# Performance work log

Hardware: AMD Instinct MI355X
Metric: run time of the kernel (lower is better)

## Reference

```python
import jax, jax.numpy as jnp
import numpy as np

N, D, H = 4096, 1024, 8
HD = D // H
FFN = int(D * 1.5)
TAU_NEG = 0.6
BETA = 1.5
LN_EPS = 1e-5


def _layernorm(x, g, b):
    mu = jnp.mean(x, axis=-1, keepdims=True)
    var = jnp.mean((x - mu) ** 2, axis=-1, keepdims=True)
    return (x - mu) * jax.lax.rsqrt(var + LN_EPS) * g + b


def setup_inputs() -> dict:
    key = jax.random.key(0)
    ks = jax.random.split(key, 16)
    s = 0.02
    inp = {
        "features": jax.random.normal(ks[0], (N, D), jnp.float32),
        "coords": jax.random.randint(ks[1], (N, 2), 0, 128, jnp.int32),
        "Wq": jax.random.normal(ks[2], (D, D), jnp.float32) * s,
        "Wk": jax.random.normal(ks[3], (D, D), jnp.float32) * s,
        "Wv": jax.random.normal(ks[4], (D, D), jnp.float32) * s,
        "Wo": jax.random.normal(ks[5], (D, D), jnp.float32) * s,
        "bo": jnp.zeros((D,), jnp.float32),
        "ln1_g": jnp.ones((D,), jnp.float32),
        "ln1_b": jnp.zeros((D,), jnp.float32),
        "W1": jax.random.normal(ks[6], (FFN, D), jnp.float32) * s,
        "b1": jnp.zeros((FFN,), jnp.float32),
        "W2": jax.random.normal(ks[7], (D, FFN), jnp.float32) * s,
        "b2": jnp.zeros((D,), jnp.float32),
        "ln2_g": jnp.ones((D,), jnp.float32),
        "ln2_b": jnp.zeros((D,), jnp.float32),
    }
    return inp


def reference(features, coords, Wq, Wk, Wv, Wo, bo, ln1_g, ln1_b, W1, b1, W2, b2, ln2_g, ln2_b):
    # QKV projections (torch Linear: x @ W.T), reshape to [H, N, HD]
    Q = (features @ Wq.T).reshape(N, H, HD).transpose(1, 0, 2)
    K = (features @ Wk.T).reshape(N, H, HD).transpose(1, 0, 2)
    V = (features @ Wv.T).reshape(N, H, HD).transpose(1, 0, 2)

    scores = jnp.einsum('hnd,hmd->hnm', Q, K) / jnp.sqrt(jnp.float32(HD))  # [H,N,N]

    # spatial distance bias from barcode coords, scaled per head by 1/2^(h+1)
    c = coords.astype(jnp.float32)
    diff = c[:, None, :] - c[None, :, :]
    dist = jnp.sqrt(jnp.sum(diff ** 2, axis=-1))  # [N,N]
    head_scalings = 1.0 / (2.0 ** (jnp.arange(1, H + 1, dtype=jnp.float32)))
    bias = dist[None, :, :] * head_scalings[:, None, None]  # [H,N,N]

    attn_pos = jax.nn.softmax(scores - bias, axis=-1)
    attn_neg = jax.nn.softmax((-scores - bias) / TAU_NEG, axis=-1)
    attn = attn_pos - BETA * attn_neg  # dropout is identity in eval

    attended = jnp.einsum('hnm,hmd->hnd', attn, V)  # [H,N,HD]
    attended = attended.transpose(1, 0, 2).reshape(N, D)

    x = attended @ Wo.T + bo + features
    x = _layernorm(x, ln1_g, ln1_b)

    h = jax.nn.gelu(x @ W1.T + b1, approximate=False)  # torch default GELU = exact erf
    ffn_out = h @ W2.T + b2
    return _layernorm(ffn_out + x, ln2_g, ln2_b)
```

## Files before the change

### kernel.cpp

```cpp
#include <hip/hip_runtime.h>
#include <cstdint>
#include <cstddef>

#define NTOK 4096
#define DMODEL 1024
#define NHEAD 8
#define DHEAD 128
#define DFFN 1536
#define LNEPS 1e-5f

typedef __bf16 bf16_t;
typedef __bf16 bf16x8 __attribute__((ext_vector_type(8)));
typedef __bf16 bf16x4 __attribute__((ext_vector_type(4)));
typedef float f32x4 __attribute__((ext_vector_type(4)));
typedef float f32x16 __attribute__((ext_vector_type(16)));

__device__ __forceinline__ void gload_lds16(const bf16_t* g, bf16_t* lds) {
  __builtin_amdgcn_global_load_lds(
      (const __attribute__((address_space(1))) unsigned int*)g,
      (__attribute__((address_space(3))) unsigned int*)lds, 16, 0, 0);
}

__device__ __forceinline__ float fexp2(float x) {
  float r;
  asm("v_exp_f32 %0, %1" : "=v"(r) : "v"(x));
  return r;
}
__device__ __forceinline__ float fsqrt(float x) {
  float r;
  asm("v_sqrt_f32 %0, %1" : "=v"(r) : "v"(x));
  return r;
}
__device__ __forceinline__ unsigned cvtpk(float lo, float hi) {
  unsigned r;
  asm("v_cvt_pk_bf16_f32 %0, %1, %2" : "=v"(r) : "v"(lo), "v"(hi));
  return r;
}

__global__ __launch_bounds__(256) void cvt_kernel(const float* __restrict__ in,
                                                  bf16_t* __restrict__ out, int n4) {
  int i = blockIdx.x * 256 + threadIdx.x;
  if (i < n4) {
    const float4 v = reinterpret_cast<const float4*>(in)[i];
    bf16x4 o = {(bf16_t)v.x, (bf16_t)v.y, (bf16_t)v.z, (bf16_t)v.w};
    reinterpret_cast<bf16x4*>(out)[i] = o;
  }
}

__global__ __launch_bounds__(256) void cvtc_kernel(const int* __restrict__ in,
                                                   float2* __restrict__ out, int n) {
  int i = blockIdx.x * 256 + threadIdx.x;
  if (i < n) {
    int2 c = reinterpret_cast<const int2*>(in)[i];
    out[i] = make_float2((float)c.x, (float)c.y);
  }
}

template<int EPI>
__global__ __launch_bounds__(256) void gemm_bt(
    const bf16_t* __restrict__ A, const bf16_t* __restrict__ B,
    int M, int Nn, int K,
    const float* __restrict__ bias, const float* __restrict__ resid,
    float* __restrict__ outF, bf16_t* __restrict__ outH)
{
  __shared__ bf16_t As[64 * 32];
  __shared__ bf16_t Bs[128 * 32];
  const int t = threadIdx.x;
  const int w = t >> 6, l = t & 63;
  const int lg = l >> 4, li = l & 15;
  const int m0 = blockIdx.x * 64, n0 = blockIdx.y * 128;
  const int wr = (w >> 1) * 32, wc = (w & 1) * 64;
  const f32x4 fz = {0.f, 0.f, 0.f, 0.f};
  f32x4 acc[2][4];
#pragma unroll
  for (int i = 0; i < 2; i++)
#pragma unroll
    for (int j = 0; j < 4; j++) acc[i][j] = fz;

  const bf16_t* Ag = A + (size_t)m0 * K;
  const bf16_t* Bg = B + (size_t)n0 * K;

  for (int kt = 0; kt < K; kt += 32) {
    if (kt) __syncthreads();
    {
      int c = w * 64 + l;
      gload_lds16(Ag + (size_t)(c >> 2) * K + kt + (c & 3) * 8,
                  As + (w * 64) * 8);
#pragma unroll
      for (int p = 0; p < 2; p++) {
        int cb = p * 256 + w * 64 + l;
        gload_lds16(Bg + (size_t)(cb >> 2) * K + kt + (cb & 3) * 8,
                    Bs + (p * 256 + w * 64) * 8);
      }
    }
    __syncthreads();
    bf16x8 af[2], bfr[4];
#pragma unroll
    for (int mi = 0; mi < 2; mi++)
      af[mi] = *reinterpret_cast<const bf16x8*>(&As[(wr + mi * 16 + li) * 32 + lg * 8]);
#pragma unroll
    for (int ni = 0; ni < 4; ni++)
      bfr[ni] = *reinterpret_cast<const bf16x8*>(&Bs[(wc + ni * 16 + li) * 32 + lg * 8]);
#pragma unroll
    for (int mi = 0; mi < 2; mi++)
#pragma unroll
      for (int ni = 0; ni < 4; ni++)
        acc[mi][ni] = __builtin_amdgcn_mfma_f32_16x16x32_bf16(af[mi], bfr[ni], acc[mi][ni], 0, 0, 0);
  }

#pragma unroll
  for (int mi = 0; mi < 2; mi++) {
#pragma unroll
    for (int ni = 0; ni < 4; ni++) {
      int gcol = n0 + wc + ni * 16 + li;
#pragma unroll
      for (int r = 0; r < 4; r++) {
        int grow = m0 + wr + mi * 16 + lg * 4 + r;
        float v = acc[mi][ni][r];
        if (EPI == 0) {
          outH[(size_t)grow * Nn + gcol] = (bf16_t)v;
        } else if (EPI == 1) {
          v += bias[gcol] + resid[(size_t)grow * Nn + gcol];
          outF[(size_t)grow * Nn + gcol] = v;
        } else if (EPI == 2) {
          v += bias[gcol];
          v = 0.5f * v * (1.f + erff(v * 0.70710678118654752f));
          outH[(size_t)grow * Nn + gcol] = (bf16_t)v;
        } else {
          v += bias[gcol] + resid[(size_t)grow * Nn + gcol];
          outF[(size_t)grow * Nn + gcol] = v;
        }
      }
    }
  }
}

__global__ __launch_bounds__(256) void packkv_kernel(
    const bf16_t* __restrict__ K, const bf16_t* __restrict__ V,
    bf16_t* __restrict__ Kp, bf16_t* __restrict__ Vp)
{
  const int h = blockIdx.x & 7;
  const int T = blockIdx.x >> 3;
  const int t = threadIdx.x;
  const size_t obase = ((size_t)(h * 128 + T)) * 4096;
#pragma unroll
  for (int rep = 0; rep < 2; rep++) {
    int idx = rep * 256 + t;
    int frag = idx >> 6, l = idx & 63;
    int q5 = l & 31, hi = l >> 5;
    bf16x8 kk = *reinterpret_cast<const bf16x8*>(
        K + (size_t)(T * 32 + q5) * DMODEL + h * DHEAD + frag * 16 + hi * 8);
    *reinterpret_cast<bf16x8*>(Kp + obase + (size_t)idx * 8) = kk;
    int ks = frag >> 2, f = frag & 3;
    bf16x8 vv;
#pragma unroll
    for (int j = 0; j < 8; j++)
      vv[j] = V[(size_t)(T * 32 + ks * 16 + hi * 8 + j) * DMODEL + h * DHEAD + 32 * f + q5];
    *reinterpret_cast<bf16x8*>(Vp + obase + (size_t)idx * 8) = vv;
  }
}

__global__ __launch_bounds__(128, 2) void attn9_kernel(
    const bf16_t* __restrict__ Q, const bf16_t* __restrict__ Kp,
    const bf16_t* __restrict__ Vp, const float2* __restrict__ cf,
    bf16_t* __restrict__ out)
{
  __shared__ float buf[128 * 33];
  __shared__ float mlS[2][32];

  const int t = threadIdx.x;
  const int w = t >> 6;
  const int l = t & 63;
  const int q5 = l & 31;
  const int hi = l >> 5;
  const int h = blockIdx.x & 7;
  const int q0 = (blockIdx.x >> 3) * 32;
  const float LOG2E = 1.44269504088896f;
  const float isq = 0.08838834764831845f;
  const float itau = 1.6666666666666667f;
  const float hs = 1.0f / (float)(2 << h);
  const float ap = isq * LOG2E;
  const float an = -isq * itau * LOG2E;
  const float bpp = hs * LOG2E;

  bf16x8 qf[8];
  {
    const bf16_t* qrow = Q + (size_t)(q0 + q5) * DMODEL + h * DHEAD;
#pragma unroll
    for (int c = 0; c < 8; c++)
      qf[c] = *reinterpret_cast<const bf16x8*>(qrow + c * 16 + hi * 8);
  }
  const float2 qc = cf[q0 + q5];
  const float qxs = qc.x * bpp, qys = qc.y * bpp;

  f32x16 accp[4], accn[4];
#pragma unroll
  for (int f = 0; f < 4; f++) {
#pragma unroll
    for (int r = 0; r < 16; r++) { accp[f][r] = 0.f; accn[f][r] = 0.f; }
  }
  float lp = 0.f, lN = 0.f;

  const bf16_t* kpb = Kp + ((size_t)(h * 128 + w * 64)) * 4096 + l * 8;
  const bf16_t* vpb = Vp + ((size_t)(h * 128 + w * 64)) * 4096 + l * 8;

  for (int it = 0; it < 64; it++) {
    const int kv0 = w * 2048 + it * 32;

    bf16x8 kf[8];
#pragma unroll
    for (int c = 0; c < 8; c++)
      kf[c] = *reinterpret_cast<const bf16x8*>(kpb + (size_t)it * 4096 + c * 512);

    f32x16 sacc, sacc2;
#pragma unroll
    for (int r = 0; r < 16; r++) { sacc[r] = 0.f; sacc2[r] = 0.f; }
#pragma unroll
    for (int c = 0; c < 4; c++) {
      sacc = __builtin_amdgcn_mfma_f32_32x32x16_bf16(kf[2 * c], qf[2 * c], sacc, 0, 0, 0);
      sacc2 = __builtin_amdgcn_mfma_f32_32x32x16_bf16(kf[2 * c + 1], qf[2 * c + 1], sacc2, 0, 0, 0);
    }

    bf16x8 vf[8];
#pragma unroll
    for (int fr = 0; fr < 8; fr++)
      vf[fr] = *reinterpret_cast<const bf16x8*>(vpb + (size_t)it * 4096 + fr * 512);

#pragma unroll
    for (int r = 0; r < 16; r++) sacc[r] += sacc2[r];

    float p16[16], n16[16];
#pragma unroll
    for (int r = 0; r < 16; r++) {
      int kvr = kv0 + (r & 3) + 8 * (r >> 2) + 4 * hi;
      float2 c = cf[kvr];
      float dx = __builtin_fmaf(c.x, -bpp, qxs);
      float dy = __builtin_fmaf(c.y, -bpp, qys);
      float u = fsqrt(__builtin_fmaf(dy, dy, dx * dx));
      float pv = fexp2(__builtin_fmaf(sacc[r], ap, -u));
      float nv = fexp2(__builtin_fmaf(sacc[r], an, u * -itau));
      p16[r] = pv; n16[r] = nv;
      lp += pv; lN += nv;
    }

    unsigned pw[2][4], nw[2][4];
#pragma unroll
    for (int ks = 0; ks < 2; ks++) {
#pragma unroll
      for (int u = 0; u < 2; u++) {
        unsigned A = cvtpk(p16[8 * ks + 2 * u], p16[8 * ks + 2 * u + 1]);
        unsigned B = cvtpk(p16[8 * ks + 4 + 2 * u], p16[8 * ks + 4 + 2 * u + 1]);
        unsigned Ax = __shfl_xor(A, 32, 64);
        unsigned Bx = __shfl_xor(B, 32, 64);
        pw[ks][u] = hi ? Bx : A;
        pw[ks][2 + u] = hi ? B : Ax;
        unsigned C = cvtpk(n16[8 * ks + 2 * u], n16[8 * ks + 2 * u + 1]);
        unsigned D = cvtpk(n16[8 * ks + 4 + 2 * u], n16[8 * ks + 4 + 2 * u + 1]);
        unsigned Cx = __shfl_xor(C, 32, 64);
        unsigned Dx = __shfl_xor(D, 32, 64);
        nw[ks][u] = hi ? Dx : C;
        nw[ks][2 + u] = hi ? D : Cx;
      }
    }

#pragma unroll
    for (int ks = 0; ks < 2; ks++) {
      union { unsigned u[4]; bf16x8 v; } pb, nb;
#pragma unroll
      for (int j = 0; j < 4; j++) { pb.u[j] = pw[ks][j]; nb.u[j] = nw[ks][j]; }
#pragma unroll
      for (int f = 0; f < 4; f++) {
        accp[f] = __builtin_amdgcn_mfma_f32_32x32x16_bf16(vf[ks * 4 + f], pb.v, accp[f], 0, 0, 0);
        accn[f] = __builtin_amdgcn_mfma_f32_32x32x16_bf16(vf[ks * 4 + f], nb.v, accn[f], 0, 0, 0);
      }
    }
  }

  float lpw = lp + __shfl_xor(lp, 32, 64);
  float lnw = lN + __shfl_xor(lN, 32, 64);

  __syncthreads();
  if (w == 1) {
    if (hi == 0) { mlS[0][q5] = lpw; mlS[1][q5] = lnw; }
#pragma unroll
    for (int f = 0; f < 4; f++)
#pragma unroll
      for (int r = 0; r < 16; r++)
        buf[(32 * f + (r & 3) + 8 * (r >> 2) + 4 * hi) * 33 + q5] = accp[f][r];
  }
  __syncthreads();
  float lpt = 0.f, lnt = 0.f;
  if (w == 0) {
    lpt = lpw + mlS[0][q5];
    lnt = lnw + mlS[1][q5];
#pragma unroll
    for (int f = 0; f < 4; f++)
#pragma unroll
      for (int r = 0; r < 16; r++)
        accp[f][r] += buf[(32 * f + (r & 3) + 8 * (r >> 2) + 4 * hi) * 33 + q5];
  }
  __syncthreads();
  if (w == 1) {
#pragma unroll
    for (int f = 0; f < 4; f++)
#pragma unroll
      for (int r = 0; r < 16; r++)
        buf[(32 * f + (r & 3) + 8 * (r >> 2) + 4 * hi) * 33 + q5] = accn[f][r];
  }
  __syncthreads();
  if (w == 0) {
    float ip = 1.f / lpt, inn = 1.5f / lnt;
#pragma unroll
    for (int f = 0; f < 4; f++)
#pragma unroll
      for (int r = 0; r < 16; r++) {
        int row = 32 * f + (r & 3) + 8 * (r >> 2) + 4 * hi;
        float an2 = accn[f][r] + buf[row * 33 + q5];
        buf[row * 33 + q5] = accp[f][r] * ip - an2 * inn;
      }
  }
  __syncthreads();

  {
    int q = t >> 2, dq = (t & 3) * 32;
#pragma unroll
    for (int j = 0; j < 4; j++) {
      bf16x8 ov;
#pragma unroll
      for (int e = 0; e < 8; e++) ov[e] = (bf16_t)buf[(dq + j * 8 + e) * 33 + q];
      *reinterpret_cast<bf16x8*>(out + (size_t)(q0 + q) * DMODEL + h * DHEAD + dq + j * 8) = ov;
    }
  }
}

__global__ __launch_bounds__(256) void ln_kernel(
    const float* __restrict__ in, const float* __restrict__ g, const float* __restrict__ b,
    float* __restrict__ outF, bf16_t* __restrict__ outH)
{
  int row = blockIdx.x, t = threadIdx.x;
  const float4 v = reinterpret_cast<const float4*>(in + (size_t)row * DMODEL)[t];
  float s = v.x + v.y + v.z + v.w;
  float ss = v.x * v.x + v.y * v.y + v.z * v.z + v.w * v.w;
#pragma unroll
  for (int m = 32; m >= 1; m >>= 1) {
    s += __shfl_xor(s, m, 64);
    ss += __shfl_xor(ss, m, 64);
  }
  __shared__ float red[8];
  int w = t >> 6, l = t & 63;
  if (l == 0) { red[w] = s; red[4 + w] = ss; }
  __syncthreads();
  s = red[0] + red[1] + red[2] + red[3];
  ss = red[4] + red[5] + red[6] + red[7];
  float mu = s * (1.f / DMODEL);
  float var = ss * (1.f / DMODEL) - mu * mu;
  float rs = rsqrtf(var + LNEPS);
  const float4 gv = reinterpret_cast<const float4*>(g)[t];
  const float4 bv = reinterpret_cast<const float4*>(b)[t];
  float y0 = (v.x - mu) * rs * gv.x + bv.x;
  float y1 = (v.y - mu) * rs * gv.y + bv.y;
  float y2 = (v.z - mu) * rs * gv.z + bv.z;
  float y3 = (v.w - mu) * rs * gv.w + bv.w;
  if (outF) {
    float4 o; o.x = y0; o.y = y1; o.z = y2; o.w = y3;
    reinterpret_cast<float4*>(outF + (size_t)row * DMODEL)[t] = o;
  }
  if (outH) {
    bf16x4 o = {(bf16_t)y0, (bf16_t)y1, (bf16_t)y2, (bf16_t)y3};
    reinterpret_cast<bf16x4*>(outH + (size_t)row * DMODEL)[t] = o;
  }
}

extern "C" void kernel_launch(void* const* d_in, const int* in_sizes, int n_in,
                              void* d_out, int out_size, void* d_ws, size_t ws_size,
                              hipStream_t stream) {
  (void)in_sizes; (void)n_in; (void)out_size; (void)ws_size;
  const float* features = (const float*)d_in[0];
  const int* coords = (const int*)d_in[1];
  const float* Wq = (const float*)d_in[2];
  const float* Wk = (const float*)d_in[3];
  const float* Wv = (const float*)d_in[4];
  const float* Wo = (const float*)d_in[5];
  const float* bo = (const float*)d_in[6];
  const float* ln1g = (const float*)d_in[7];
  const float* ln1b = (const float*)d_in[8];
  const float* W1 = (const float*)d_in[9];
  const float* b1 = (const float*)d_in[10];
  const float* W2 = (const float*)d_in[11];
  const float* b2 = (const float*)d_in[12];
  const float* ln2g = (const float*)d_in[13];
  const float* ln2b = (const float*)d_in[14];
  float* outp = (float*)d_out;

  char* ws = (char*)d_ws;
  size_t off = 0;
  auto alloc = [&](size_t bytes) -> void* {
    void* p = ws + off;
    off += (bytes + 255) & ~((size_t)255);
    return p;
  };
  bf16_t* fb16 = (bf16_t*)alloc((size_t)NTOK * DMODEL * 2);
  bf16_t* wq16 = (bf16_t*)alloc((size_t)DMODEL * DMODEL * 2);
  bf16_t* wk16 = (bf16_t*)alloc((size_t)DMODEL * DMODEL * 2);
  bf16_t* wv16 = (bf16_t*)alloc((size_t)DMODEL * DMODEL * 2);
  bf16_t* wo16 = (bf16_t*)alloc((size_t)DMODEL * DMODEL * 2);
  bf16_t* w116 = (bf16_t*)alloc((size_t)DFFN * DMODEL * 2);
  bf16_t* w216 = (bf16_t*)alloc((size_t)DMODEL * DFFN * 2);
  bf16_t* q16 = (bf16_t*)alloc((size_t)NTOK * DMODEL * 2);
  bf16_t* k16 = (bf16_t*)alloc((size_t)NTOK * DMODEL * 2);
  bf16_t* v16 = (bf16_t*)alloc((size_t)NTOK * DMODEL * 2);
  float* acc1 = (float*)alloc((size_t)NTOK * DMODEL * 4);
  float* xf = (float*)alloc((size_t)NTOK * DMODEL * 4);
  bf16_t* x16 = (bf16_t*)alloc((size_t)NTOK * DMODEL * 2);
  bf16_t* h16 = (bf16_t*)alloc((size_t)NTOK * DFFN * 2);
  float2* cfl = (float2*)alloc((size_t)NTOK * sizeof(float2));
  bf16_t* att16 = fb16;
  bf16_t* Kp = (bf16_t*)acc1;
  bf16_t* Vp = (bf16_t*)h16;

  cvt_kernel<<<dim3(NTOK * DMODEL / 1024), 256, 0, stream>>>(features, fb16, NTOK * DMODEL / 4);
  cvt_kernel<<<dim3(DMODEL * DMODEL / 1024), 256, 0, stream>>>(Wq, wq16, DMODEL * DMODEL / 4);
  cvt_kernel<<<dim3(DMODEL * DMODEL / 1024), 256, 0, stream>>>(Wk, wk16, DMODEL * DMODEL / 4);
  cvt_kernel<<<dim3(DMODEL * DMODEL / 1024), 256, 0, stream>>>(Wv, wv16, DMODEL * DMODEL / 4);
  cvt_kernel<<<dim3(DMODEL * DMODEL / 1024), 256, 0, stream>>>(Wo, wo16, DMODEL * DMODEL / 4);
  cvt_kernel<<<dim3(DFFN * DMODEL / 1024), 256, 0, stream>>>(W1, w116, DFFN * DMODEL / 4);
  cvt_kernel<<<dim3(DMODEL * DFFN / 1024), 256, 0, stream>>>(W2, w216, DMODEL * DFFN / 4);
  cvtc_kernel<<<dim3(NTOK / 256), 256, 0, stream>>>(coords, cfl, NTOK);

  dim3 gQKV(NTOK / 64, DMODEL / 128);
  gemm_bt<0><<<gQKV, 256, 0, stream>>>(fb16, wq16, NTOK, DMODEL, DMODEL, nullptr, nullptr, nullptr, q16);
  gemm_bt<0><<<gQKV, 256, 0, stream>>>(fb16, wk16, NTOK, DMODEL, DMODEL, nullptr, nullptr, nullptr, k16);
  gemm_bt<0><<<gQKV, 256, 0, stream>>>(fb16, wv16, NTOK, DMODEL, DMODEL, nullptr, nullptr, nullptr, v16);
  packkv_kernel<<<dim3(NTOK / 32 * NHEAD), 256, 0, stream>>>(k16, v16, Kp, Vp);
  attn9_kernel<<<dim3(NTOK / 32 * NHEAD), 128, 0, stream>>>(q16, Kp, Vp, cfl, att16);
  gemm_bt<1><<<gQKV, 256, 0, stream>>>(att16, wo16, NTOK, DMODEL, DMODEL, bo, features, acc1, nullptr);
  ln_kernel<<<dim3(NTOK), 256, 0, stream>>>(acc1, ln1g, ln1b, xf, x16);
  gemm_bt<2><<<dim3(NTOK / 64, DFFN / 128), 256, 0, stream>>>(x16, w116, NTOK, DFFN, DMODEL, b1, nullptr, nullptr, h16);
  gemm_bt<3><<<gQKV, 256, 0, stream>>>(h16, w216, NTOK, DMODEL, DFFN, b2, xf, acc1, nullptr);
  ln_kernel<<<dim3(NTOK), 256, 0, stream>>>(acc1, ln2g, ln2b, outp, nullptr);
}
```

Before: 340.9 us.

## Fuse QKV GEMMs with K/V packing epilogue and double-buffer GEMM LDS

Concatenates Wq/Wk/Wv into one weight buffer and runs a single QKV GEMM whose epilogue writes Q row-major and scatters K and V straight into the packed per-head layouts the attention kernel expects. This removes the separate packkv pass and its extra read and write of K and V. All GEMMs also get double-buffered LDS tiles, so the next K-slice load can overlap the MFMA work on the current one. In exchange, the epilogue stores become scattered scalar writes, LDS use doubles, and Kp/Vp now get their own workspace instead of aliasing acc1 and h16.

```diff
diff --git a/kernel.cpp b/kernel.cpp
--- a/kernel.cpp
+++ b/kernel.cpp
@@ -63,8 +63,8 @@
     const float* __restrict__ bias, const float* __restrict__ resid,
     float* __restrict__ outF, bf16_t* __restrict__ outH)
 {
-  __shared__ bf16_t As[64 * 32];
-  __shared__ bf16_t Bs[128 * 32];
+  __shared__ bf16_t As[2][64 * 32];
+  __shared__ bf16_t Bs[2][128 * 32];
   const int t = threadIdx.x;
   const int w = t >> 6, l = t & 63;
   const int lg = l >> 4, li = l & 15;
@@ -79,33 +79,43 @@
 
   const bf16_t* Ag = A + (size_t)m0 * K;
   const bf16_t* Bg = B + (size_t)n0 * K;
-
-  for (int kt = 0; kt < K; kt += 32) {
-    if (kt) __syncthreads();
-    {
-      int c = w * 64 + l;
-      gload_lds16(Ag + (size_t)(c >> 2) * K + kt + (c & 3) * 8,
-                  As + (w * 64) * 8);
+  const int ca = w * 64 + l;
+  const int nK = K >> 5;
+
+  gload_lds16(Ag + (size_t)(ca >> 2) * K + (ca & 3) * 8, &As[0][(w * 64) * 8]);
+#pragma unroll
+  for (int p = 0; p < 2; p++) {
+    int cb = p * 256 + ca;
+    gload_lds16(Bg + (size_t)(cb >> 2) * K + (cb & 3) * 8, &Bs[0][(p * 256 + w * 64) * 8]);
+  }
+  __syncthreads();
+
+  for (int ki = 0; ki < nK; ki++) {
+    const int cur = ki & 1;
+    if (ki + 1 < nK) {
+      const int kt = (ki + 1) << 5;
+      gload_lds16(Ag + (size_t)(ca >> 2) * K + kt + (ca & 3) * 8,
+                  &As[cur ^ 1][(w * 64) * 8]);
 #pragma unroll
       for (int p = 0; p < 2; p++) {
-        int cb = p * 256 + w * 64 + l;
+        int cb = p * 256 + ca;
         gload_lds16(Bg + (size_t)(cb >> 2) * K + kt + (cb & 3) * 8,
-                    Bs + (p * 256 + w * 64) * 8);
-      }
-    }
-    __syncthreads();
+                    &Bs[cur ^ 1][(p * 256 + w * 64) * 8]);
+      }
+    }
     bf16x8 af[2], bfr[4];
 #pragma unroll
     for (int mi = 0; mi < 2; mi++)
-      af[mi] = *reinterpret_cast<const bf16x8*>(&As[(wr + mi * 16 + li) * 32 + lg * 8]);
+      af[mi] = *reinterpret_cast<const bf16x8*>(&As[cur][(wr + mi * 16 + li) * 32 + lg * 8]);
 #pragma unroll
     for (int ni = 0; ni < 4; ni++)
-      bfr[ni] = *reinterpret_cast<const bf16x8*>(&Bs[(wc + ni * 16 + li) * 32 + lg * 8]);
+      bfr[ni] = *reinterpret_cast<const bf16x8*>(&Bs[cur][(wc + ni * 16 + li) * 32 + lg * 8]);
 #pragma unroll
     for (int mi = 0; mi < 2; mi++)
 #pragma unroll
       for (int ni = 0; ni < 4; ni++)
         acc[mi][ni] = __builtin_amdgcn_mfma_f32_16x16x32_bf16(af[mi], bfr[ni], acc[mi][ni], 0, 0, 0);
+    __syncthreads();
   }
 
 #pragma unroll
@@ -135,28 +145,94 @@
   }
 }
 
-__global__ __launch_bounds__(256) void packkv_kernel(
-    const bf16_t* __restrict__ K, const bf16_t* __restrict__ V,
-    bf16_t* __restrict__ Kp, bf16_t* __restrict__ Vp)
+__global__ __launch_bounds__(256) void gemm_qkv(
+    const bf16_t* __restrict__ A, const bf16_t* __restrict__ B,
+    bf16_t* __restrict__ Qo, bf16_t* __restrict__ Kp, bf16_t* __restrict__ Vp)
 {
-  const int h = blockIdx.x & 7;
-  const int T = blockIdx.x >> 3;
+  const int K = DMODEL;
+  __shared__ bf16_t As[2][64 * 32];
+  __shared__ bf16_t Bs[2][128 * 32];
   const int t = threadIdx.x;
-  const size_t obase = ((size_t)(h * 128 + T)) * 4096;
-#pragma unroll
-  for (int rep = 0; rep < 2; rep++) {
-    int idx = rep * 256 + t;
-    int frag = idx >> 6, l = idx & 63;
-    int q5 = l & 31, hi = l >> 5;
-    bf16x8 kk = *reinterpret_cast<const bf16x8*>(
-        K + (size_t)(T * 32 + q5) * DMODEL + h * DHEAD + frag * 16 + hi * 8);
-    *reinterpret_cast<bf16x8*>(Kp + obase + (size_t)idx * 8) = kk;
-    int ks = frag >> 2, f = frag & 3;
-    bf16x8 vv;
-#pragma unroll
-    for (int j = 0; j < 8; j++)
-      vv[j] = V[(size_t)(T * 32 + ks * 16 + hi * 8 + j) * DMODEL + h * DHEAD + 32 * f + q5];
-    *reinterpret_cast<bf16x8*>(Vp + obase + (size_t)idx * 8) = vv;
+  const int w = t >> 6, l = t & 63;
+  const int lg = l >> 4, li = l & 15;
+  const int m0 = blockIdx.x * 64, n0 = blockIdx.y * 128;
+  const int wr = (w >> 1) * 32, wc = (w & 1) * 64;
+  const f32x4 fz = {0.f, 0.f, 0.f, 0.f};
+  f32x4 acc[2][4];
+#pragma unroll
+  for (int i = 0; i < 2; i++)
+#pragma unroll
+    for (int j = 0; j < 4; j++) acc[i][j] = fz;
+
+  const bf16_t* Ag = A + (size_t)m0 * K;
+  const bf16_t* Bg = B + (size_t)n0 * K;
+  const int ca = w * 64 + l;
+  const int nK = K >> 5;
+
+  gload_lds16(Ag + (size_t)(ca >> 2) * K + (ca & 3) * 8, &As[0][(w * 64) * 8]);
+#pragma unroll
+  for (int p = 0; p < 2; p++) {
+    int cb = p * 256 + ca;
+    gload_lds16(Bg + (size_t)(cb >> 2) * K + (cb & 3) * 8, &Bs[0][(p * 256 + w * 64) * 8]);
+  }
+  __syncthreads();
+
+  for (int ki = 0; ki < nK; ki++) {
+    const int cur = ki & 1;
+    if (ki + 1 < nK) {
+      const int kt = (ki + 1) << 5;
+      gload_lds16(Ag + (size_t)(ca >> 2) * K + kt + (ca & 3) * 8,
+                  &As[cur ^ 1][(w * 64) * 8]);
+#pragma unroll
+      for (int p = 0; p < 2; p++) {
+        int cb = p * 256 + ca;
+        gload_lds16(Bg + (size_t)(cb >> 2) * K + kt + (cb & 3) * 8,
+                    &Bs[cur ^ 1][(p * 256 + w * 64) * 8]);
+      }
+    }
+    bf16x8 af[2], bfr[4];
+#pragma unroll
+    for (int mi = 0; mi < 2; mi++)
+      af[mi] = *reinterpret_cast<const bf16x8*>(&As[cur][(wr + mi * 16 + li) * 32 + lg * 8]);
+#pragma unroll
+    for (int ni = 0; ni < 4; ni++)
+      bfr[ni] = *reinterpret_cast<const bf16x8*>(&Bs[cur][(wc + ni * 16 + li) * 32 + lg * 8]);
+#pragma unroll
+    for (int mi = 0; mi < 2; mi++)
+#pragma unroll
+      for (int ni = 0; ni < 4; ni++)
+        acc[mi][ni] = __builtin_amdgcn_mfma_f32_16x16x32_bf16(af[mi], bfr[ni], acc[mi][ni], 0, 0, 0);
+    __syncthreads();
+  }
+
+  const int region = n0 >> 10;
+#pragma unroll
+  for (int mi = 0; mi < 2; mi++) {
+#pragma unroll
+    for (int ni = 0; ni < 4; ni++) {
+      int gcol = n0 + wc + ni * 16 + li;
+#pragma unroll
+      for (int r = 0; r < 4; r++) {
+        int token = m0 + wr + mi * 16 + lg * 4 + r;
+        bf16_t v = (bf16_t)acc[mi][ni][r];
+        if (region == 0) {
+          Qo[(size_t)token * DMODEL + gcol] = v;
+        } else if (region == 1) {
+          int gc = gcol - 1024;
+          int h = gc >> 7, d = gc & 127;
+          size_t addr = ((size_t)(h * 128 + (token >> 5))) * 4096 +
+                        (d >> 4) * 512 + ((d >> 3) & 1) * 256 + (token & 31) * 8 + (d & 7);
+          Kp[addr] = v;
+        } else {
+          int gc = gcol - 2048;
+          int h = gc >> 7, dh = gc & 127;
+          size_t addr = ((size_t)(h * 128 + (token >> 5))) * 4096 +
+                        (((token >> 4) & 1) * 4 + (dh >> 5)) * 512 +
+                        ((token >> 3) & 1) * 256 + (dh & 31) * 8 + (token & 7);
+          Vp[addr] = v;
+        }
+      }
+    }
   }
 }
 
@@ -400,42 +476,35 @@
     return p;
   };
   bf16_t* fb16 = (bf16_t*)alloc((size_t)NTOK * DMODEL * 2);
-  bf16_t* wq16 = (bf16_t*)alloc((size_t)DMODEL * DMODEL * 2);
-  bf16_t* wk16 = (bf16_t*)alloc((size_t)DMODEL * DMODEL * 2);
-  bf16_t* wv16 = (bf16_t*)alloc((size_t)DMODEL * DMODEL * 2);
+  bf16_t* wqkv16 = (bf16_t*)alloc((size_t)3 * DMODEL * DMODEL * 2);
   bf16_t* wo16 = (bf16_t*)alloc((size_t)DMODEL * DMODEL * 2);
   bf16_t* w116 = (bf16_t*)alloc((size_t)DFFN * DMODEL * 2);
   bf16_t* w216 = (bf16_t*)alloc((size_t)DMODEL * DFFN * 2);
   bf16_t* q16 = (bf16_t*)alloc((size_t)NTOK * DMODEL * 2);
-  bf16_t* k16 = (bf16_t*)alloc((size_t)NTOK * DMODEL * 2);
-  bf16_t* v16 = (bf16_t*)alloc((size_t)NTOK * DMODEL * 2);
+  bf16_t* Kp = (bf16_t*)alloc((size_t)NTOK * DMODEL * 2);
+  bf16_t* Vp = (bf16_t*)alloc((size_t)NTOK * DMODEL * 2);
   float* acc1 = (float*)alloc((size_t)NTOK * DMODEL * 4);
   float* xf = (float*)alloc((size_t)NTOK * DMODEL * 4);
   bf16_t* x16 = (bf16_t*)alloc((size_t)NTOK * DMODEL * 2);
   bf16_t* h16 = (bf16_t*)alloc((size_t)NTOK * DFFN * 2);
   float2* cfl = (float2*)alloc((size_t)NTOK * sizeof(float2));
   bf16_t* att16 = fb16;
-  bf16_t* Kp = (bf16_t*)acc1;
-  bf16_t* Vp = (bf16_t*)h16;
 
   cvt_kernel<<<dim3(NTOK * DMODEL / 1024), 256, 0, stream>>>(features, fb16, NTOK * DMODEL / 4);
-  cvt_kernel<<<dim3(DMODEL * DMODEL / 1024), 256, 0, stream>>>(Wq, wq16, DMODEL * DMODEL / 4);
-  cvt_kernel<<<dim3(DMODEL * DMODEL / 1024), 256, 0, stream>>>(Wk, wk16, DMODEL * DMODEL / 4);
-  cvt_kernel<<<dim3(DMODEL * DMODEL / 1024), 256, 0, stream>>>(Wv, wv16, DMODEL * DMODEL / 4);
+  cvt_kernel<<<dim3(DMODEL * DMODEL / 1024), 256, 0, stream>>>(Wq, wqkv16, DMODEL * DMODEL / 4);
+  cvt_kernel<<<dim3(DMODEL * DMODEL / 1024), 256, 0, stream>>>(Wk, wqkv16 + (size_t)DMODEL * DMODEL, DMODEL * DMODEL / 4);
+  cvt_kernel<<<dim3(DMODEL * DMODEL / 1024), 256, 0, stream>>>(Wv, wqkv16 + (size_t)2 * DMODEL * DMODEL, DMODEL * DMODEL / 4);
   cvt_kernel<<<dim3(DMODEL * DMODEL / 1024), 256, 0, stream>>>(Wo, wo16, DMODEL * DMODEL / 4);
   cvt_kernel<<<dim3(DFFN * DMODEL / 1024), 256, 0, stream>>>(W1, w116, DFFN * DMODEL / 4);
   cvt_kernel<<<dim3(DMODEL * DFFN / 1024), 256, 0, stream>>>(W2, w216, DMODEL * DFFN / 4);
   cvtc_kernel<<<dim3(NTOK / 256), 256, 0, stream>>>(coords, cfl, NTOK);
 
-  dim3 gQKV(NTOK / 64, DMODEL / 128);
-  gemm_bt<0><<<gQKV, 256, 0, stream>>>(fb16, wq16, NTOK, DMODEL, DMODEL, nullptr, nullptr, nullptr, q16);
-  gemm_bt<0><<<gQKV, 256, 0, stream>>>(fb16, wk16, NTOK, DMODEL, DMODEL, nullptr, nullptr, nullptr, k16);
-  gemm_bt<0><<<gQKV, 256, 0, stream>>>(fb16, wv16, NTOK, DMODEL, DMODEL, nullptr, nullptr, nullptr, v16);
-  packkv_kernel<<<dim3(NTOK / 32 * NHEAD), 256, 0, stream>>>(k16, v16, Kp, Vp);
+  gemm_qkv<<<dim3(NTOK / 64, 3 * DMODEL / 128), 256, 0, stream>>>(fb16, wqkv16, q16, Kp, Vp);
   attn9_kernel<<<dim3(NTOK / 32 * NHEAD), 128, 0, stream>>>(q16, Kp, Vp, cfl, att16);
-  gemm_bt<1><<<gQKV, 256, 0, stream>>>(att16, wo16, NTOK, DMODEL, DMODEL, bo, features, acc1, nullptr);
+  dim3 gO(NTOK / 64, DMODEL / 128);
+  gemm_bt<1><<<gO, 256, 0, stream>>>(att16, wo16, NTOK, DMODEL, DMODEL, bo, features, acc1, nullptr);
   ln_kernel<<<dim3(NTOK), 256, 0, stream>>>(acc1, ln1g, ln1b, xf, x16);
   gemm_bt<2><<<dim3(NTOK / 64, DFFN / 128), 256, 0, stream>>>(x16, w116, NTOK, DFFN, DMODEL, b1, nullptr, nullptr, h16);
-  gemm_bt<3><<<gQKV, 256, 0, stream>>>(h16, w216, NTOK, DMODEL, DFFN, b2, xf, acc1, nullptr);
+  gemm_bt<3><<<gO, 256, 0, stream>>>(h16, w216, NTOK, DMODEL, DFFN, b2, xf, acc1, nullptr);
   ln_kernel<<<dim3(NTOK), 256, 0, stream>>>(acc1, ln2g, ln2b, outp, nullptr);
 }
```

Result: faster. 329.8 us (-3.3%).
